# Kernel tuning notes

Hardware: AMD Instinct MI355X
Metric: run time of the kernel (lower is better)

Reference implementation:

```python
import jax, jax.numpy as jnp
import numpy as np

# ProjectorConfig defaults
MIN_SPEECH_FRAMES = 1.0
MAX_SPEECH_EXPAND = 3.0
TAIL_HOLD_UNITS = 2
BOUNDARY_COMMIT_THRESHOLD = 0.45

B, U = 4096, 2048


def setup_inputs() -> dict:
    key = jax.random.key(0)
    ks = jax.random.split(key, 10)
    # ragged prefix mask: random visible length per row (faithful to streaming use)
    lengths = jax.random.randint(ks[0], (B,), 1, U + 1)
    unit_mask = (jnp.arange(U)[None, :] < lengths[:, None]).astype(jnp.float32)
    dur_anchor_src = jax.random.uniform(ks[1], (B, U), jnp.float32) * 20.0
    dur_logratio_unit = jax.random.normal(ks[2], (B, U), jnp.float32) * 0.3
    pause_weight_unit = jax.random.uniform(ks[3], (B, U), jnp.float32)
    boundary_latent = jax.random.uniform(ks[4], (B, U), jnp.float32)
    speech_budget_win = jax.random.uniform(ks[5], (B, 1), jnp.float32) * float(U) * 10.0
    pause_budget_win = jax.random.uniform(ks[6], (B, 1), jnp.float32) * float(U)
    open_run_mask = jax.random.bernoulli(ks[7], 0.1, (B, U)).astype(jnp.int32)
    return {
        "dur_anchor_src": dur_anchor_src,
        "unit_mask": unit_mask,
        "speech_budget_win": speech_budget_win,
        "pause_budget_win": pause_budget_win,
        "dur_logratio_unit": dur_logratio_unit,
        "pause_weight_unit": pause_weight_unit,
        "boundary_latent": boundary_latent,
        "phase_ptr": jnp.zeros((B,), jnp.float32),
        "backlog": jnp.zeros((B,), jnp.float32),
        "clock_delta": jnp.zeros((B,), jnp.float32),
        "commit_frontier": jnp.zeros((B,), jnp.int32),
        "open_run_mask": open_run_mask,
    }


def reference(dur_anchor_src, unit_mask, speech_budget_win, pause_budget_win,
              dur_logratio_unit, pause_weight_unit, boundary_latent,
              phase_ptr, backlog, clock_delta, commit_frontier, open_run_mask):
    b, u = unit_mask.shape

    # ---- _project_speech ----
    anchor = jnp.maximum(dur_anchor_src, MIN_SPEECH_FRAMES)
    base = anchor * jnp.exp(dur_logratio_unit)
    speech = jnp.maximum(jnp.minimum(base, anchor * MAX_SPEECH_EXPAND), MIN_SPEECH_FRAMES) * unit_mask
    total = jnp.maximum((speech * unit_mask).sum(axis=1, keepdims=True), 1e-6)
    speech = speech * (speech_budget_win / total) * unit_mask

    # ---- _project_pause ----
    scores = jnp.maximum(pause_weight_unit, 0.0) * (0.5 + boundary_latent) * unit_mask
    score_total = scores.sum(axis=1, keepdims=True)
    fallback = unit_mask / jnp.maximum(unit_mask.sum(axis=1, keepdims=True), 1.0)
    weights = jnp.where(score_total > 0, scores / jnp.maximum(score_total, 1e-6), fallback)
    pause = weights * pause_budget_win

    effective = (speech + pause) * unit_mask

    # ---- _compute_commit_frontier (vectorized) ----
    visible = unit_mask.sum(axis=1).astype(jnp.int32)                 # active_len [B]
    idx = jnp.arange(u, dtype=jnp.int32)[None, :]
    open_vis = (open_run_mask > 0) & (idx < visible[:, None])
    has_open = open_vis.any(axis=1)
    first_open = jnp.argmax(open_vis, axis=1).astype(jnp.int32)
    closed_prefix = jnp.where(has_open, first_open, visible)          # leading closed run
    release_cap = jnp.maximum(visible - TAIL_HOLD_UNITS, 0)
    candidate = jnp.minimum(release_cap, closed_prefix)
    prev = commit_frontier.astype(jnp.int32)
    b_idx = jnp.clip(candidate - 1, 0, u - 1)
    b_val = jnp.take_along_axis(boundary_latent, b_idx[:, None], axis=1)[:, 0]
    soft = (candidate > 0) & (candidate < visible) & (b_val < BOUNDARY_COMMIT_THRESHOLD)
    candidate = jnp.where(soft, jnp.maximum(prev, candidate - 1), candidate)
    commit = jnp.maximum(prev, candidate)

    # ---- _advance_state (prefix sums instead of python loops) ----
    zeros_col = jnp.zeros((b, 1), effective.dtype)
    cs_eff = jnp.concatenate([zeros_col, jnp.cumsum(effective, axis=1)], axis=1)
    cs_src = jnp.concatenate([zeros_col, jnp.cumsum(dur_anchor_src, axis=1)], axis=1)
    take = lambda cs, i: jnp.take_along_axis(cs, i[:, None], axis=1)[:, 0]
    exec_prefix = take(cs_eff, commit) - take(cs_eff, prev)
    src_prefix = take(cs_src, commit) - take(cs_src, prev)
    adv = commit > prev
    delta = exec_prefix - src_prefix
    next_clock = jnp.where(adv, clock_delta + delta, clock_delta)
    next_backlog = jnp.where(adv, jnp.maximum(next_clock, 0.0), backlog)
    visible_total = jnp.maximum(effective.sum(axis=1), 1.0)
    next_phase = jnp.where(adv, jnp.clip(phase_ptr + exec_prefix / visible_total, 0.0, 1.0), phase_ptr)

    return (speech, pause, effective, commit, next_phase, next_backlog, next_clock)
```

## Files before the change

### kernel.cpp

```cpp
#include <hip/hip_runtime.h>
#include <climits>


constexpr int UNITS = 2048;
constexpr int BLOCK = 64;
constexpr int CH = UNITS / (BLOCK * 4);

static __device__ __forceinline__ float bflySum(float v) {
#pragma unroll
  for (int m = 1; m < 64; m <<= 1) v += __shfl_xor(v, m, 64);
  return v;
}
static __device__ __forceinline__ int bflyMin(int v) {
#pragma unroll
  for (int m = 1; m < 64; m <<= 1) v = min(v, __shfl_xor(v, m, 64));
  return v;
}

__global__ __launch_bounds__(BLOCK, 4) void rhythm_kernel(
    const float* __restrict__ dur_anchor,
    const float* __restrict__ unit_mask,
    const float* __restrict__ speech_budget,
    const float* __restrict__ pause_budget,
    const float* __restrict__ dur_logratio,
    const float* __restrict__ pause_weight,
    const float* __restrict__ boundary,
    const float* __restrict__ phase_ptr,
    const float* __restrict__ backlog,
    const float* __restrict__ clock_delta,
    const int*   __restrict__ commit_front,
    const int*   __restrict__ open_run,
    float* __restrict__ out,
    int B) {
  const int row = blockIdx.x;
  const int t = threadIdx.x;
  const size_t base = (size_t)row * UNITS;

  const int prev = commit_front[row];
  const float sb = speech_budget[row];
  const float pb = pause_budget[row];
  const float pp = phase_ptr[row];
  const float bl = backlog[row];
  const float cd = clock_delta[row];

  float sv_sr[CH * 4];
  float sv_src[CH * 4];
  float sum_sr = 0.f, sum_sc = 0.f, sum_m = 0.f;
  int min_open = INT_MAX;

#pragma unroll
  for (int c = 0; c < CH; ++c) {
    const int e0 = c * (BLOCK * 4) + 4 * t;
    const float4 a4 = *(const float4*)(dur_anchor   + base + e0);
    const float4 m4 = *(const float4*)(unit_mask    + base + e0);
    const float4 l4 = *(const float4*)(dur_logratio + base + e0);
    const float4 p4 = *(const float4*)(pause_weight + base + e0);
    const float4 b4 = *(const float4*)(boundary     + base + e0);
    const int4   o4 = *(const int4*)(open_run       + base + e0);
    const float av[4] = {a4.x, a4.y, a4.z, a4.w};
    const float mv[4] = {m4.x, m4.y, m4.z, m4.w};
    const float lv[4] = {l4.x, l4.y, l4.z, l4.w};
    const float pv[4] = {p4.x, p4.y, p4.z, p4.w};
    const float bv[4] = {b4.x, b4.y, b4.z, b4.w};
    const int   ov[4] = {o4.x, o4.y, o4.z, o4.w};
#pragma unroll
    for (int j = 0; j < 4; ++j) {
      const int k = c * 4 + j;
      const float m = mv[j];
      const float a = fmaxf(av[j], 1.0f);
      const float bse = a * __expf(lv[j]);
      const float sr = fmaxf(fminf(bse, 3.0f * a), 1.0f) * m;
      const float sc = fmaxf(pv[j], 0.0f) * (0.5f + bv[j]) * m;
      sv_sr[k] = sr;
      sv_src[k] = av[j];
      sum_sr += sr;
      sum_sc += sc;
      sum_m += m;
      if (ov[j] > 0 && m > 0.5f) min_open = min(min_open, e0 + j);
    }
  }

  const float ts = bflySum(sum_sr);
  const float tc = bflySum(sum_sc);
  const float tm = bflySum(sum_m);
  const int mo = bflyMin(min_open);

  const int visible = (int)(tm + 0.5f);
  const int closed = (mo == INT_MAX) ? visible : mo;
  const int relcap = max(visible - 2, 0);
  int cand = min(relcap, closed);
  const int bidx = min(max(cand - 1, 0), UNITS - 1);
  const float bval = boundary[base + bidx];
  if (cand > 0 && cand < visible && bval < 0.45f)
    cand = max(prev, cand - 1);
  const int commit = max(prev, cand);

  const float sscale = sb / fmaxf(ts, 1e-6f);
  const bool usefb = !(tc > 0.0f);
  const float pscale = pb / fmaxf(tc, 1e-6f);
  const float fbw = pb / fmaxf(tm, 1.0f);

  float* __restrict__ out_speech = out;
  float* __restrict__ out_pause  = out + (size_t)B * UNITS;
  float* __restrict__ out_eff    = out + 2 * (size_t)B * UNITS;

  float eff_rng = 0.f, src_rng = 0.f, eff_tot = 0.f;
#pragma unroll
  for (int c = 0; c < CH; ++c) {
    const int e0 = c * (BLOCK * 4) + 4 * t;
    const float4 p4 = *(const float4*)(pause_weight + base + e0);
    const float4 b4 = *(const float4*)(boundary     + base + e0);
    const float pv[4] = {p4.x, p4.y, p4.z, p4.w};
    const float bv[4] = {b4.x, b4.y, b4.z, b4.w};
    float s_[4], q_[4], e_[4];
#pragma unroll
    for (int j = 0; j < 4; ++j) {
      const int k = c * 4 + j;
      const int idx = e0 + j;
      const float sr = sv_sr[k];
      const float m = (sr != 0.0f) ? 1.0f : 0.0f;
      const float sc = fmaxf(pv[j], 0.0f) * (0.5f + bv[j]) * m;
      const float speech = sr * sscale;
      const float pause = usefb ? (m * fbw) : (sc * pscale);
      const float eff = (speech + pause) * m;
      s_[j] = speech;
      q_[j] = pause;
      e_[j] = eff;
      eff_tot += eff;
      const bool inr = (idx >= prev) && (idx < commit);
      eff_rng += inr ? eff : 0.f;
      src_rng += inr ? sv_src[k] : 0.f;
    }
    *reinterpret_cast<float4*>(out_speech + base + e0) =
        make_float4(s_[0], s_[1], s_[2], s_[3]);
    *reinterpret_cast<float4*>(out_pause + base + e0) =
        make_float4(q_[0], q_[1], q_[2], q_[3]);
    *reinterpret_cast<float4*>(out_eff + base + e0) =
        make_float4(e_[0], e_[1], e_[2], e_[3]);
  }

  const float execp = bflySum(eff_rng);
  const float srcp = bflySum(src_rng);
  const float etot = bflySum(eff_tot);

  if (t == 0) {
    const bool adv = commit > prev;
    const float nclock = adv ? (cd + (execp - srcp)) : cd;
    const float nback = adv ? fmaxf(nclock, 0.0f) : bl;
    const float vt = fmaxf(etot, 1.0f);
    const float nphase =
        adv ? fminf(fmaxf(pp + execp / vt, 0.0f), 1.0f) : pp;
    const size_t o = 3 * (size_t)B * UNITS;
    out[o + row] = (float)commit;
    out[o + (size_t)B + row] = nphase;
    out[o + 2 * (size_t)B + row] = nback;
    out[o + 3 * (size_t)B + row] = nclock;
  }
}

extern "C" void kernel_launch(void* const* d_in, const int* in_sizes, int n_in,
                              void* d_out, int out_size, void* d_ws, size_t ws_size,
                              hipStream_t stream) {
  const int B = in_sizes[7];
  rhythm_kernel<<<dim3(B), dim3(BLOCK), 0, stream>>>(
      (const float*)d_in[0],
      (const float*)d_in[1],
      (const float*)d_in[2],
      (const float*)d_in[3],
      (const float*)d_in[4],
      (const float*)d_in[5],
      (const float*)d_in[6],
      (const float*)d_in[7],
      (const float*)d_in[8],
      (const float*)d_in[9],
      (const int*)d_in[10],
      (const int*)d_in[11],
      (float*)d_out, B);
}
```

Before: 294.9 us.

## Use 256-thread blocks with LDS reductions, cache pause scores, nontemporal stores

Each row is now handled by four waves of 256 threads instead of one wave, so every thread holds 8 elements instead of 32, and partial sums are combined through shared memory with a barrier. The per-element pause score is kept in registers, so pause_weight and boundary are not read a second time. The effective-duration total is computed in closed form from the scale factors, and the source-duration prefix is summed with a strided loop over only the committed range. Output stores use nontemporal hints. The costs are two block barriers and a change in floating-point summation order for the total, which may differ slightly from the reference.

```diff
diff --git a/kernel.cpp b/kernel.cpp
--- a/kernel.cpp
+++ b/kernel.cpp
@@ -3,15 +3,17 @@
 
 
 constexpr int UNITS = 2048;
-constexpr int BLOCK = 64;
-constexpr int CH = UNITS / (BLOCK * 4);
+constexpr int BLOCK = 256;
+constexpr int EPT = UNITS / BLOCK;
 
-static __device__ __forceinline__ float bflySum(float v) {
+typedef float f32x4 __attribute__((ext_vector_type(4)));
+
+static __device__ __forceinline__ float waveSum(float v) {
 #pragma unroll
   for (int m = 1; m < 64; m <<= 1) v += __shfl_xor(v, m, 64);
   return v;
 }
-static __device__ __forceinline__ int bflyMin(int v) {
+static __device__ __forceinline__ int waveMin(int v) {
 #pragma unroll
   for (int m = 1; m < 64; m <<= 1) v = min(v, __shfl_xor(v, m, 64));
   return v;
@@ -43,13 +45,13 @@
   const float bl = backlog[row];
   const float cd = clock_delta[row];
 
-  float sv_sr[CH * 4];
-  float sv_src[CH * 4];
+  float sv_sr[EPT];
+  float sv_sc[EPT];
   float sum_sr = 0.f, sum_sc = 0.f, sum_m = 0.f;
   int min_open = INT_MAX;
 
 #pragma unroll
-  for (int c = 0; c < CH; ++c) {
+  for (int c = 0; c < EPT / 4; ++c) {
     const int e0 = c * (BLOCK * 4) + 4 * t;
     const float4 a4 = *(const float4*)(dur_anchor   + base + e0);
     const float4 m4 = *(const float4*)(unit_mask    + base + e0);
@@ -72,7 +74,7 @@
       const float sr = fmaxf(fminf(bse, 3.0f * a), 1.0f) * m;
       const float sc = fmaxf(pv[j], 0.0f) * (0.5f + bv[j]) * m;
       sv_sr[k] = sr;
-      sv_src[k] = av[j];
+      sv_sc[k] = sc;
       sum_sr += sr;
       sum_sc += sc;
       sum_m += m;
@@ -80,10 +82,22 @@
     }
   }
 
-  const float ts = bflySum(sum_sr);
-  const float tc = bflySum(sum_sc);
-  const float tm = bflySum(sum_m);
-  const int mo = bflyMin(min_open);
+  const int wv = t >> 6, ln = t & 63;
+  __shared__ float sf[3][4];
+  __shared__ int si[4];
+  __shared__ float sg[2][4];
+
+  const float r0 = waveSum(sum_sr);
+  const float r1 = waveSum(sum_sc);
+  const float r2 = waveSum(sum_m);
+  const int ri = waveMin(min_open);
+  if (ln == 0) { sf[0][wv] = r0; sf[1][wv] = r1; sf[2][wv] = r2; si[wv] = ri; }
+  __syncthreads();
+
+  const float ts = sf[0][0] + sf[0][1] + sf[0][2] + sf[0][3];
+  const float tc = sf[1][0] + sf[1][1] + sf[1][2] + sf[1][3];
+  const float tm = sf[2][0] + sf[2][1] + sf[2][2] + sf[2][3];
+  const int mo = min(min(si[0], si[1]), min(si[2], si[3]));
 
   const int visible = (int)(tm + 0.5f);
   const int closed = (mo == INT_MAX) ? visible : mo;
@@ -99,55 +113,52 @@
   const bool usefb = !(tc > 0.0f);
   const float pscale = pb / fmaxf(tc, 1e-6f);
   const float fbw = pb / fmaxf(tm, 1.0f);
+  const float eff_tot = usefb ? (sscale * ts + fbw * tm) : (sscale * ts + pscale * tc);
+
+  float src_rng = 0.f;
+  for (int i = prev + t; i < commit; i += BLOCK) src_rng += dur_anchor[base + i];
 
   float* __restrict__ out_speech = out;
   float* __restrict__ out_pause  = out + (size_t)B * UNITS;
   float* __restrict__ out_eff    = out + 2 * (size_t)B * UNITS;
 
-  float eff_rng = 0.f, src_rng = 0.f, eff_tot = 0.f;
+  float eff_rng = 0.f;
 #pragma unroll
-  for (int c = 0; c < CH; ++c) {
+  for (int c = 0; c < EPT / 4; ++c) {
     const int e0 = c * (BLOCK * 4) + 4 * t;
-    const float4 p4 = *(const float4*)(pause_weight + base + e0);
-    const float4 b4 = *(const float4*)(boundary     + base + e0);
-    const float pv[4] = {p4.x, p4.y, p4.z, p4.w};
-    const float bv[4] = {b4.x, b4.y, b4.z, b4.w};
-    float s_[4], q_[4], e_[4];
+    f32x4 s4, q4, e4;
 #pragma unroll
     for (int j = 0; j < 4; ++j) {
       const int k = c * 4 + j;
       const int idx = e0 + j;
       const float sr = sv_sr[k];
       const float m = (sr != 0.0f) ? 1.0f : 0.0f;
-      const float sc = fmaxf(pv[j], 0.0f) * (0.5f + bv[j]) * m;
       const float speech = sr * sscale;
-      const float pause = usefb ? (m * fbw) : (sc * pscale);
+      const float pause = usefb ? (m * fbw) : (sv_sc[k] * pscale);
       const float eff = (speech + pause) * m;
-      s_[j] = speech;
-      q_[j] = pause;
-      e_[j] = eff;
-      eff_tot += eff;
+      s4[j] = speech;
+      q4[j] = pause;
+      e4[j] = eff;
       const bool inr = (idx >= prev) && (idx < commit);
       eff_rng += inr ? eff : 0.f;
-      src_rng += inr ? sv_src[k] : 0.f;
     }
-    *reinterpret_cast<float4*>(out_speech + base + e0) =
-        make_float4(s_[0], s_[1], s_[2], s_[3]);
-    *reinterpret_cast<float4*>(out_pause + base + e0) =
-        make_float4(q_[0], q_[1], q_[2], q_[3]);
-    *reinterpret_cast<float4*>(out_eff + base + e0) =
-        make_float4(e_[0], e_[1], e_[2], e_[3]);
+    __builtin_nontemporal_store(s4, (f32x4*)(out_speech + base + e0));
+    __builtin_nontemporal_store(q4, (f32x4*)(out_pause + base + e0));
+    __builtin_nontemporal_store(e4, (f32x4*)(out_eff + base + e0));
   }
 
-  const float execp = bflySum(eff_rng);
-  const float srcp = bflySum(src_rng);
-  const float etot = bflySum(eff_tot);
+  const float q0 = waveSum(eff_rng);
+  const float q1 = waveSum(src_rng);
+  if (ln == 0) { sg[0][wv] = q0; sg[1][wv] = q1; }
+  __syncthreads();
 
   if (t == 0) {
+    const float execp = sg[0][0] + sg[0][1] + sg[0][2] + sg[0][3];
+    const float srcp  = sg[1][0] + sg[1][1] + sg[1][2] + sg[1][3];
     const bool adv = commit > prev;
     const float nclock = adv ? (cd + (execp - srcp)) : cd;
     const float nback = adv ? fmaxf(nclock, 0.0f) : bl;
-    const float vt = fmaxf(etot, 1.0f);
+    const float vt = fmaxf(eff_tot, 1.0f);
     const float nphase =
         adv ? fminf(fmaxf(pp + execp / vt, 0.0f), 1.0f) : pp;
     const size_t o = 3 * (size_t)B * UNITS;
```

Measured after the change: 265.6 us. -9.9%, faster.
